# Performance work log

Hardware: AMD Instinct MI355X
Metric: run time of the kernel (lower is better)

The kernel has to match this reference:

```python
import jax, jax.numpy as jnp
import numpy as np

B, C, STRIDE = 2, 2048, 8
N = C * STRIDE            # sequence_length = 16384
D, H, L, FF = 256, 8, 4, 2048
DH = D // H


def setup_inputs() -> dict:
    key = jax.random.key(0)
    ks = iter(jax.random.split(key, 40))
    init = lambda shape: jax.random.normal(next(ks), shape, jnp.float32) * 0.02
    inp = {
        'bucket_tokens': jax.random.normal(next(ks), (B, C, STRIDE), jnp.float32),
        'W_in': init((STRIDE, D)), 'b_in': jnp.zeros((D,), jnp.float32),
        'Wq': init((L, D, D)), 'bq': jnp.zeros((L, D), jnp.float32),
        'Wk': init((L, D, D)), 'bk': jnp.zeros((L, D), jnp.float32),
        'Wv': init((L, D, D)), 'bv': jnp.zeros((L, D), jnp.float32),
        'Wo': init((L, D, D)), 'bo': jnp.zeros((L, D), jnp.float32),
        'ln1_g': jnp.ones((L, D), jnp.float32), 'ln1_b': jnp.zeros((L, D), jnp.float32),
        'ln2_g': jnp.ones((L, D), jnp.float32), 'ln2_b': jnp.zeros((L, D), jnp.float32),
        'W1': init((L, D, FF)), 'b1': jnp.zeros((L, FF), jnp.float32),
        'W2': init((L, FF, D)), 'b2': jnp.zeros((L, D), jnp.float32),
        'W_out': init((D, N)), 'b_out': jnp.zeros((N,), jnp.float32),
        'k_tokens': 60,  # int(fast_k * log(C)) = int(8 * log(2048))
    }
    return inp


def _layernorm(x, g, b, eps=1e-5):
    mu = x.mean(-1, keepdims=True)
    var = ((x - mu) ** 2).mean(-1, keepdims=True)
    return (x - mu) * jax.lax.rsqrt(var + eps) * g + b


def _rope_tables(seq, dh, dtype):
    half = dh // 2
    inv_freq = 1.0 / (10000.0 ** (jnp.arange(half, dtype=dtype) / half))
    ang = jnp.arange(seq, dtype=dtype)[:, None] * inv_freq[None, :]  # [C, half]
    return jnp.cos(ang), jnp.sin(ang)


def _apply_rope(t, cos, sin):
    # t: [B, H, C, DH]; rotate-half convention
    half = t.shape[-1] // 2
    t1, t2 = t[..., :half], t[..., half:]
    return jnp.concatenate([t1 * cos - t2 * sin, t1 * sin + t2 * cos], axis=-1)


def reference(bucket_tokens, W_in, b_in, Wq, bq, Wk, bk, Wv, bv, Wo, bo,
              ln1_g, ln1_b, ln2_g, ln2_b, W1, b1, W2, b2, W_out, b_out, k_tokens):
    x = bucket_tokens @ W_in + b_in                               # [B, C, D]
    dtype = x.dtype
    # ring-causal local mask: query c attends to {c, c-1, ..., c-(k-1)} mod C
    idx = jnp.arange(C)
    dist = (idx[:, None] - idx[None, :]) % C                       # [C, C]
    allowed = dist < k_tokens
    bias = jnp.where(allowed, jnp.zeros((), dtype), jnp.finfo(dtype).min)  # [C, C]
    cos, sin = _rope_tables(C, DH, dtype)
    scale = 1.0 / jnp.sqrt(jnp.asarray(DH, dtype))

    def heads(t):  # [B, C, D] -> [B, H, C, DH]
        return t.reshape(B, C, H, DH).transpose(0, 2, 1, 3)

    for l in range(L):
        h = _layernorm(x, ln1_g[l], ln1_b[l])
        q = _apply_rope(heads(h @ Wq[l] + bq[l]), cos, sin)
        k = _apply_rope(heads(h @ Wk[l] + bk[l]), cos, sin)
        v = heads(h @ Wv[l] + bv[l])
        scores = jnp.einsum('bhqd,bhkd->bhqk', q, k) * scale + bias
        attn = jax.nn.softmax(scores, axis=-1)
        o = jnp.einsum('bhqk,bhkd->bhqd', attn, v)
        o = o.transpose(0, 2, 1, 3).reshape(B, C, D)
        x = x + o @ Wo[l] + bo[l]
        h2 = _layernorm(x, ln2_g[l], ln2_b[l])
        x = x + jax.nn.relu(h2 @ W1[l] + b1[l]) @ W2[l] + b2[l]
    return x @ W_out + b_out                                       # [B, C, N]
```

## Files before the change

kernel.cpp:

```cpp
#include <hip/hip_runtime.h>
#include <hip/hip_bf16.h>

typedef __hip_bfloat16 bf16;
typedef float f32x4 __attribute__((ext_vector_type(4)));
typedef __bf16 bf16x8 __attribute__((ext_vector_type(8)));
typedef unsigned short u16x8 __attribute__((ext_vector_type(8)));
typedef unsigned short u16x4 __attribute__((ext_vector_type(4)));

#define FLAG_RELU  1
#define FLAG_OBF16 2
#define FLAG_RESID 4
#define FLAG_ROPE  8
#define FLAG_ATOM  16

__device__ __forceinline__ void glds16(const void* g, void* l) {
  __builtin_amdgcn_global_load_lds((const __attribute__((address_space(1))) void*)g,
                                   (__attribute__((address_space(3))) void*)l, 16, 0, 0);
}

__device__ __forceinline__ float ldf(const void* p, size_t i, bool f32) {
  return f32 ? ((const float*)p)[i] : (float)((const bf16*)p)[i];
}

__device__ __forceinline__ float bf2f(unsigned short u) {
  return __uint_as_float((unsigned)u << 16);
}
__device__ __forceinline__ short f2s(float f) {
  bf16 b = __float2bfloat16(f);
  return *(short*)&b;
}

__global__ void detect_k(const unsigned short* ln1g, int* flag) {
  *flag = (ln1g[0] == 0) ? 1 : 0;
}

__global__ __launch_bounds__(256) void transpose_k(const void* __restrict__ in,
                                                   bf16* __restrict__ out, int R, int Ccols,
                                                   const int* __restrict__ flag) {
  const bool f32 = *flag != 0;
  __shared__ bf16 tile[32][33];
  const size_t mz = (size_t)blockIdx.z * R * Ccols;
  const int c0 = blockIdx.x * 32, r0 = blockIdx.y * 32;
  const int tx = threadIdx.x & 31, ty = threadIdx.x >> 5;
#pragma unroll
  for (int i = 0; i < 32; i += 8)
    tile[ty + i][tx] = __float2bfloat16(ldf(in, mz + (size_t)(r0 + ty + i) * Ccols + c0 + tx, f32));
  __syncthreads();
#pragma unroll
  for (int i = 0; i < 32; i += 8)
    out[mz + (size_t)(c0 + ty + i) * R + r0 + tx] = tile[tx][ty + i];
}

__global__ __launch_bounds__(256) void inproj_k(const void* __restrict__ toks,
                                                const void* __restrict__ Win,
                                                const void* __restrict__ bin,
                                                float* __restrict__ x,
                                                const int* __restrict__ flag) {
  const bool f32 = *flag != 0;
  const int t = blockIdx.x, d = threadIdx.x;
  float acc = ldf(bin, d, f32);
#pragma unroll
  for (int s = 0; s < 8; s++)
    acc += ldf(toks, (size_t)t * 8 + s, f32) * ldf(Win, s * 256 + d, f32);
  x[(size_t)t * 256 + d] = acc;
}

__global__ __launch_bounds__(256) void ln_k(const float* __restrict__ x,
                                            const void* __restrict__ g,
                                            const void* __restrict__ bta, int eoff,
                                            bf16* __restrict__ out,
                                            const int* __restrict__ flag) {
  const bool f32 = *flag != 0;
  const int lane = threadIdx.x & 63;
  const size_t t = (size_t)blockIdx.x * 4 + (threadIdx.x >> 6);
  const float4 v = *(const float4*)(x + t * 256 + lane * 4);
  float s = v.x + v.y + v.z + v.w;
#pragma unroll
  for (int o = 32; o > 0; o >>= 1) s += __shfl_xor(s, o);
  const float mu = s * 0.00390625f;
  const float dx = v.x - mu, dy = v.y - mu, dz = v.z - mu, dw = v.w - mu;
  float ss = dx * dx + dy * dy + dz * dz + dw * dw;
#pragma unroll
  for (int o = 32; o > 0; o >>= 1) ss += __shfl_xor(ss, o);
  const float r = rsqrtf(ss * 0.00390625f + 1e-5f);
  const int e = eoff + lane * 4;
  short4 o4;
  o4.x = f2s(dx * r * ldf(g, e + 0, f32) + ldf(bta, e + 0, f32));
  o4.y = f2s(dy * r * ldf(g, e + 1, f32) + ldf(bta, e + 1, f32));
  o4.z = f2s(dz * r * ldf(g, e + 2, f32) + ldf(bta, e + 2, f32));
  o4.w = f2s(dw * r * ldf(g, e + 3, f32) + ldf(bta, e + 3, f32));
  *(short4*)((short*)out + t * 256 + lane * 4) = o4;
}

__global__ __launch_bounds__(256) void attn_k(const bf16* __restrict__ q,
                                              const bf16* __restrict__ k,
                                              const bf16* __restrict__ v,
                                              bf16* __restrict__ out,
                                              const int* __restrict__ ktp) {
  __shared__ unsigned short ksu[64][40];
  __shared__ unsigned short vsu[64][40];
  __shared__ float ps[32][40];
  int iv = *ktp;
  int kt;
  if (iv >= 1 && iv <= 2048) kt = iv;
  else {
    float fv = __int_as_float(iv);
    kt = (fv >= 1.0f && fv < 2049.0f) ? (int)fv : 60;
  }
  const int t = threadIdx.x;
  const int q0 = blockIdx.x * 32;
  const int h = blockIdx.y & 7, b = blockIdx.y >> 3;
  const size_t base_bh = ((size_t)b * 2048) * 256 + h * 32;
  const int qi = t >> 3, g = t & 7;
  const int srow = t >> 2, sd0 = (t & 3) * 8;
  const unsigned short* kg = (const unsigned short*)k + base_bh + sd0;
  const unsigned short* vg = (const unsigned short*)v + base_bh + sd0;
  float qv[32];
  {
    const unsigned short* qg = (const unsigned short*)q + base_bh + (size_t)(q0 + qi) * 256;
#pragma unroll
    for (int c = 0; c < 4; ++c) {
      u16x8 q8 = *(const u16x8*)(qg + c * 8);
#pragma unroll
      for (int e = 0; e < 8; ++e) qv[c * 8 + e] = bf2f(q8[e]);
    }
  }
  float m_run = -3.0e38f, l_run = 0.0f;
  float acc0 = 0.f, acc1 = 0.f, acc2 = 0.f, acc3 = 0.f;
  const float scale = 0.17677669529663687f;
  const int nch = (kt + 31) >> 5;
  for (int ch = 0; ch < nch; ++ch) {
    const int jb = ch << 5;
    if (ch) __syncthreads();
    {
      const int pos = (q0 - jb - 31 + srow) & 2047;
      *(u16x8*)&ksu[srow][sd0] = *(const u16x8*)(kg + (size_t)pos * 256);
      *(u16x8*)&vsu[srow][sd0] = *(const u16x8*)(vg + (size_t)pos * 256);
    }
    __syncthreads();
    float sc[4];
    float mloc = -3.0e38f;
#pragma unroll
    for (int s4 = 0; s4 < 4; ++s4) {
      const int dj = g + 8 * s4;
      const unsigned short* kr = ksu[qi - dj + 31];
      float dot = 0.f;
#pragma unroll
      for (int c = 0; c < 4; ++c) {
        u16x8 kk = *(const u16x8*)(kr + c * 8);
#pragma unroll
        for (int e = 0; e < 8; ++e) dot += qv[c * 8 + e] * bf2f(kk[e]);
      }
      const float sv = (jb + dj < kt) ? dot * scale : -3.0e38f;
      sc[s4] = sv;
      mloc = fmaxf(mloc, sv);
    }
    mloc = fmaxf(mloc, __shfl_xor(mloc, 1));
    mloc = fmaxf(mloc, __shfl_xor(mloc, 2));
    mloc = fmaxf(mloc, __shfl_xor(mloc, 4));
    const float mnew = fmaxf(m_run, mloc);
    const float fr = expf(m_run - mnew);
    float lloc = 0.f;
#pragma unroll
    for (int s4 = 0; s4 < 4; ++s4) {
      const float pe = expf(sc[s4] - mnew);
      ps[qi][g + 8 * s4] = pe;
      lloc += pe;
    }
    lloc += __shfl_xor(lloc, 1);
    lloc += __shfl_xor(lloc, 2);
    lloc += __shfl_xor(lloc, 4);
    m_run = mnew;
    l_run = l_run * fr + lloc;
    acc0 *= fr; acc1 *= fr; acc2 *= fr; acc3 *= fr;
    __syncthreads();
#pragma unroll 8
    for (int dj = 0; dj < 32; ++dj) {
      const float pe = ps[qi][dj];
      const u16x4 vv = *(const u16x4*)&vsu[qi - dj + 31][g * 4];
      acc0 += pe * bf2f(vv[0]);
      acc1 += pe * bf2f(vv[1]);
      acc2 += pe * bf2f(vv[2]);
      acc3 += pe * bf2f(vv[3]);
    }
  }
  const float invs = (l_run > 0.f) ? 1.f / l_run : 0.f;
  short4 o4;
  o4.x = f2s(acc0 * invs);
  o4.y = f2s(acc1 * invs);
  o4.z = f2s(acc2 * invs);
  o4.w = f2s(acc3 * invs);
  *(short4*)((short*)out + base_bh + (size_t)(q0 + qi) * 256 + g * 4) = o4;
}

__global__ __launch_bounds__(256) void gemm128_k(const bf16* __restrict__ A,
                                                 const bf16* __restrict__ BT,
                                                 const void* __restrict__ bias, int boff,
                                                 const float* resid, void* out,
                                                 int K, int N, int flags,
                                                 const int* __restrict__ dflag) {
  const bool bf32 = *dflag != 0;
  __shared__ __align__(16) short As[128 * 32];
  __shared__ __align__(16) short Bs[128 * 32];
  const int t = threadIdx.x;
  const int bm = blockIdx.x, bn = blockIdx.y;
  const int w = t >> 6, lane = t & 63;
  const int wm = (w >> 1) * 64, wn = (w & 1) * 64;
  const int lr = lane & 15, lq = lane >> 4;
  const short* Ag = (const short*)A + (size_t)bm * 128 * K + (size_t)(t >> 2) * K + (t & 3) * 8;
  const short* Bg = (const short*)BT + (size_t)bn * 128 * K + (size_t)(t >> 2) * K + (t & 3) * 8;
  const size_t rowhalf = (size_t)64 * K;
  f32x4 acc[4][4] = {};
  for (int kt = 0; kt < K; kt += 32) {
    glds16(Ag + kt, &As[t * 8]);
    glds16(Ag + rowhalf + kt, &As[2048 + t * 8]);
    glds16(Bg + kt, &Bs[t * 8]);
    glds16(Bg + rowhalf + kt, &Bs[2048 + t * 8]);
    __syncthreads();
    bf16x8 af[4], bfr[4];
#pragma unroll
    for (int i = 0; i < 4; i++) af[i] = *(const bf16x8*)&As[(wm + i * 16 + lr) * 32 + lq * 8];
#pragma unroll
    for (int j = 0; j < 4; j++) bfr[j] = *(const bf16x8*)&Bs[(wn + j * 16 + lr) * 32 + lq * 8];
#pragma unroll
    for (int i = 0; i < 4; i++)
#pragma unroll
      for (int j = 0; j < 4; j++)
        acc[i][j] = __builtin_amdgcn_mfma_f32_16x16x32_bf16(af[i], bfr[j], acc[i][j], 0, 0, 0);
    __syncthreads();
  }
  const int relu = flags & FLAG_RELU, obf = flags & FLAG_OBF16, res = flags & FLAG_RESID;
#pragma unroll
  for (int i = 0; i < 4; i++) {
    const size_t row0 = (size_t)bm * 128 + wm + i * 16 + lq * 4;
#pragma unroll
    for (int j = 0; j < 4; j++) {
      const int col = bn * 128 + wn + j * 16 + lr;
      const float bb = ldf(bias, boff + col, bf32);
#pragma unroll
      for (int r = 0; r < 4; r++) {
        const size_t idx = (row0 + r) * (size_t)N + col;
        float vv = acc[i][j][r] + bb;
        if (relu) vv = fmaxf(vv, 0.0f);
        if (res) vv += resid[idx];
        if (obf) ((bf16*)out)[idx] = __float2bfloat16(vv);
        else ((float*)out)[idx] = vv;
      }
    }
  }
}

__device__ __forceinline__ void gemm64_body(const bf16* A, const bf16* BT, const void* bias,
                                            int boff, const float* resid, void* out, int K,
                                            int k0, int k1, int N, int flags, int bm, int bn,
                                            bool bf32) {
  __shared__ __align__(16) short As[64 * 32];
  __shared__ __align__(16) short Bs[64 * 32];
  const int t = threadIdx.x;
  const int w = t >> 6, lane = t & 63;
  const int wm = (w >> 1) * 32, wn = (w & 1) * 32;
  const int lr = lane & 15, lq = lane >> 4;
  const short* Ag = (const short*)A + (size_t)bm * 64 * K + (size_t)(t >> 2) * K + (t & 3) * 8;
  const short* Bg = (const short*)BT + (size_t)bn * 64 * K + (size_t)(t >> 2) * K + (t & 3) * 8;
  f32x4 acc[2][2] = {};
  for (int kt = k0; kt < k1; kt += 32) {
    glds16(Ag + kt, &As[t * 8]);
    glds16(Bg + kt, &Bs[t * 8]);
    __syncthreads();
    bf16x8 af[2], bfr[2];
#pragma unroll
    for (int i = 0; i < 2; i++) af[i] = *(const bf16x8*)&As[(wm + i * 16 + lr) * 32 + lq * 8];
#pragma unroll
    for (int j = 0; j < 2; j++) bfr[j] = *(const bf16x8*)&Bs[(wn + j * 16 + lr) * 32 + lq * 8];
#pragma unroll
    for (int i = 0; i < 2; i++)
#pragma unroll
      for (int j = 0; j < 2; j++)
        acc[i][j] = __builtin_amdgcn_mfma_f32_16x16x32_bf16(af[i], bfr[j], acc[i][j], 0, 0, 0);
    __syncthreads();
  }
  if (flags & FLAG_ROPE) {
    const int col0 = bn * 64 + wn + lr;
    const float inv = powf(10000.0f, -(float)lr * 0.0625f);
    const float b0 = ldf(bias, boff + col0, bf32);
    const float b1 = ldf(bias, boff + col0 + 16, bf32);
#pragma unroll
    for (int i = 0; i < 2; i++) {
      const int row0 = bm * 64 + wm + i * 16 + lq * 4;
#pragma unroll
      for (int r = 0; r < 4; r++) {
        const int row = row0 + r;
        const float ang = (float)(row & 2047) * inv;
        const float cc = cosf(ang), sn = sinf(ang);
        const float v0 = acc[i][0][r] + b0, v1 = acc[i][1][r] + b1;
        bf16* ob = (bf16*)out + (size_t)row * N + col0;
        ob[0]  = __float2bfloat16(v0 * cc - v1 * sn);
        ob[16] = __float2bfloat16(v0 * sn + v1 * cc);
      }
    }
    return;
  }
  if (flags & FLAG_ATOM) {
#pragma unroll
    for (int i = 0; i < 2; i++) {
      const size_t row0 = (size_t)bm * 64 + wm + i * 16 + lq * 4;
#pragma unroll
      for (int j = 0; j < 2; j++) {
        const int col = bn * 64 + wn + j * 16 + lr;
        const float bb = bias ? ldf(bias, boff + col, bf32) : 0.0f;
#pragma unroll
        for (int r = 0; r < 4; r++)
          atomicAdd((float*)out + (row0 + r) * (size_t)N + col, acc[i][j][r] + bb);
      }
    }
    return;
  }
  const int relu = flags & FLAG_RELU, obf = flags & FLAG_OBF16, res = flags & FLAG_RESID;
#pragma unroll
  for (int i = 0; i < 2; i++) {
    const size_t row0 = (size_t)bm * 64 + wm + i * 16 + lq * 4;
#pragma unroll
    for (int j = 0; j < 2; j++) {
      const int col = bn * 64 + wn + j * 16 + lr;
      const float bb = ldf(bias, boff + col, bf32);
#pragma unroll
      for (int r = 0; r < 4; r++) {
        const size_t idx = (row0 + r) * (size_t)N + col;
        float vv = acc[i][j][r] + bb;
        if (relu) vv = fmaxf(vv, 0.0f);
        if (res) vv += resid[idx];
        if (obf) ((bf16*)out)[idx] = __float2bfloat16(vv);
        else ((float*)out)[idx] = vv;
      }
    }
  }
}

__global__ __launch_bounds__(256) void gemm64_k(const bf16* __restrict__ A,
                                                const bf16* __restrict__ BT,
                                                const void* __restrict__ bias, int boff,
                                                const float* resid, void* out,
                                                int K, int N, int flags,
                                                const int* __restrict__ dflag) {
  gemm64_body(A, BT, bias, boff, resid, out, K, 0, K, N, flags, blockIdx.x, blockIdx.y,
              *dflag != 0);
}

__global__ __launch_bounds__(256) void gemm64sk_k(const bf16* __restrict__ A,
                                                  const bf16* __restrict__ BT,
                                                  const void* __restrict__ bias, int boff,
                                                  float* out, int K, int Ksl, int N,
                                                  const int* __restrict__ dflag) {
  const int z = blockIdx.z;
  gemm64_body(A, BT, z == 0 ? bias : nullptr, boff, nullptr, out, K, z * Ksl, z * Ksl + Ksl, N,
              FLAG_ATOM, blockIdx.x, blockIdx.y, *dflag != 0);
}

__global__ __launch_bounds__(256) void qkv_k(const bf16* __restrict__ A,
                                             const bf16* __restrict__ BTq, const bf16* __restrict__ BTk,
                                             const bf16* __restrict__ BTv,
                                             const void* __restrict__ biq, const void* __restrict__ bik,
                                             const void* __restrict__ biv, int boff,
                                             bf16* q, bf16* k, bf16* v, int K, int N,
                                             const int* __restrict__ dflag) {
  const bf16* BT; const void* bi; bf16* o; int fl;
  if (blockIdx.z == 0)      { BT = BTq; bi = biq; o = q; fl = FLAG_ROPE; }
  else if (blockIdx.z == 1) { BT = BTk; bi = bik; o = k; fl = FLAG_ROPE; }
  else                      { BT = BTv; bi = biv; o = v; fl = FLAG_OBF16; }
  gemm64_body(A, BT, bi, boff, nullptr, o, K, 0, K, N, fl, blockIdx.x, blockIdx.y, *dflag != 0);
}

__global__ void cast_k(const float* __restrict__ in, bf16* __restrict__ out) {
  int i = blockIdx.x * 256 + threadIdx.x;
  out[i] = __float2bfloat16(in[i]);
}

extern "C" void kernel_launch(void* const* d_in, const int* in_sizes, int n_in,
                              void* d_out, int out_size, void* d_ws, size_t ws_size,
                              hipStream_t stream) {
  (void)in_sizes; (void)n_in; (void)out_size; (void)ws_size;
  const void* toks = d_in[0];
  const void* Win  = d_in[1];
  const void* bin  = d_in[2];
  const void* Wq   = d_in[3];
  const void* bq   = d_in[4];
  const void* Wk   = d_in[5];
  const void* bk   = d_in[6];
  const void* Wv   = d_in[7];
  const void* bv   = d_in[8];
  const void* Wo   = d_in[9];
  const void* bo   = d_in[10];
  const void* ln1g = d_in[11];
  const void* ln1b = d_in[12];
  const void* ln2g = d_in[13];
  const void* ln2b = d_in[14];
  const void* W1   = d_in[15];
  const void* b1   = d_in[16];
  const void* W2   = d_in[17];
  const void* b2   = d_in[18];
  const void* Wout = d_in[19];
  const void* bout = d_in[20];
  const int*  ktp  = (const int*)d_in[21];

  char* p = (char*)d_ws;
  auto take = [&](size_t bytes) { char* r = p; p += bytes; return r; };
  int*  dflag = (int*)take(256);
  float* x    = (float*)take((size_t)4096 * 256 * 4);
  bf16* h     = (bf16*)take((size_t)4096 * 256 * 2);
  bf16* qb    = (bf16*)take((size_t)4096 * 256 * 2);
  bf16* kbb   = (bf16*)take((size_t)4096 * 256 * 2);
  bf16* vbb   = (bf16*)take((size_t)4096 * 256 * 2);
  bf16* ao    = (bf16*)take((size_t)4096 * 256 * 2);
  bf16* mid   = (bf16*)take((size_t)4096 * 2048 * 2);
  bf16* xb    = (bf16*)take((size_t)4096 * 256 * 2);
  bf16* WqT   = (bf16*)take((size_t)4 * 256 * 256 * 2);
  bf16* WkT   = (bf16*)take((size_t)4 * 256 * 256 * 2);
  bf16* WvT   = (bf16*)take((size_t)4 * 256 * 256 * 2);
  bf16* WoT   = (bf16*)take((size_t)4 * 256 * 256 * 2);
  bf16* W1T   = (bf16*)take((size_t)4 * 256 * 2048 * 2);
  bf16* W2T   = (bf16*)take((size_t)4 * 2048 * 256 * 2);
  bf16* WoutT = (bf16*)take((size_t)256 * 16384 * 2);

  detect_k<<<1, 1, 0, stream>>>((const unsigned short*)ln1g, dflag);

  transpose_k<<<dim3(8, 8, 4), 256, 0, stream>>>(Wq, WqT, 256, 256, dflag);
  transpose_k<<<dim3(8, 8, 4), 256, 0, stream>>>(Wk, WkT, 256, 256, dflag);
  transpose_k<<<dim3(8, 8, 4), 256, 0, stream>>>(Wv, WvT, 256, 256, dflag);
  transpose_k<<<dim3(8, 8, 4), 256, 0, stream>>>(Wo, WoT, 256, 256, dflag);
  transpose_k<<<dim3(64, 8, 4), 256, 0, stream>>>(W1, W1T, 256, 2048, dflag);
  transpose_k<<<dim3(8, 64, 4), 256, 0, stream>>>(W2, W2T, 2048, 256, dflag);
  transpose_k<<<dim3(512, 8, 1), 256, 0, stream>>>(Wout, WoutT, 256, 16384, dflag);

  inproj_k<<<4096, 256, 0, stream>>>(toks, Win, bin, x, dflag);

  for (int l = 0; l < 4; l++) {
    ln_k<<<1024, 256, 0, stream>>>(x, ln1g, ln1b, l * 256, h, dflag);
    qkv_k<<<dim3(64, 4, 3), 256, 0, stream>>>(h, WqT + l * 65536, WkT + l * 65536, WvT + l * 65536,
                                              bq, bk, bv, l * 256, qb, kbb, vbb, 256, 256, dflag);
    attn_k<<<dim3(64, 16), 256, 0, stream>>>(qb, kbb, vbb, ao, ktp);
    gemm64sk_k<<<dim3(64, 4, 2), 256, 0, stream>>>(ao, WoT + l * 65536, bo, l * 256, x,
                                                   256, 128, 256, dflag);
    ln_k<<<1024, 256, 0, stream>>>(x, ln2g, ln2b, l * 256, h, dflag);
    gemm128_k<<<dim3(32, 16), 256, 0, stream>>>(h, W1T + (size_t)l * 524288, b1, l * 2048, nullptr,
                                                mid, 256, 2048, FLAG_RELU | FLAG_OBF16, dflag);
    gemm64sk_k<<<dim3(64, 4, 4), 256, 0, stream>>>(mid, W2T + (size_t)l * 524288, b2, l * 256, x,
                                                   2048, 512, 256, dflag);
  }

  cast_k<<<4096, 256, 0, stream>>>(x, xb);
  gemm128_k<<<dim3(32, 128), 256, 0, stream>>>(xb, WoutT, bout, 0, nullptr, d_out,
                                               256, 16384, 0, dflag);
}
```

Before: 752.6 us.

## Merge weight transposes, fuse QKV into 128-tile GEMM, add XCD block remap

All seven weight transposes are merged into one launch, and the detect kernel is removed: each kernel now reads the dtype flag directly from ln1_g. The QKV projection moves from three 64-tile GEMM slices to one 128-tile GEMM over a concatenated QKV weight, with RoPE applied in the epilogue. The FFN down-projection now uses a split-K 128-tile GEMM with atomic adds. GEMMs also remap block ids so that neighbouring tiles land on the same XCD, which targets L2 reuse. Together these cut launch count and raise per-block MFMA work, at the cost of fewer blocks for the smaller GEMMs.

```diff
diff --git a/kernel.cpp b/kernel.cpp
--- a/kernel.cpp
+++ b/kernel.cpp
@@ -10,7 +10,6 @@
 #define FLAG_RELU  1
 #define FLAG_OBF16 2
 #define FLAG_RESID 4
-#define FLAG_ROPE  8
 #define FLAG_ATOM  16
 
 __device__ __forceinline__ void glds16(const void* g, void* l) {
@@ -30,33 +29,59 @@
   return *(short*)&b;
 }
 
-__global__ void detect_k(const unsigned short* ln1g, int* flag) {
-  *flag = (ln1g[0] == 0) ? 1 : 0;
-}
-
-__global__ __launch_bounds__(256) void transpose_k(const void* __restrict__ in,
-                                                   bf16* __restrict__ out, int R, int Ccols,
-                                                   const int* __restrict__ flag) {
-  const bool f32 = *flag != 0;
+__device__ __forceinline__ bool is_f32(const unsigned short* dt) { return dt[0] == 0; }
+
+__global__ __launch_bounds__(256) void transposeAll_k(
+    const void* __restrict__ Wq, const void* __restrict__ Wk, const void* __restrict__ Wv,
+    const void* __restrict__ Wo, const void* __restrict__ W1, const void* __restrict__ W2,
+    const void* __restrict__ Wout,
+    bf16* __restrict__ qkvT, bf16* __restrict__ WoT, bf16* __restrict__ W1T,
+    bf16* __restrict__ W2T, bf16* __restrict__ WoutT,
+    const unsigned short* __restrict__ dt) {
+  const bool f32 = is_f32(dt);
+  const int esz = f32 ? 4 : 2;
+  const int id = blockIdx.x;
+  const void* in; bf16* out; int R, C, r0, c0;
+  if (id < 1024) {
+    const int seg = id >> 8, rem = id & 255;
+    const int layer = rem >> 6, tile = rem & 63;
+    c0 = (tile & 7) * 32; r0 = (tile >> 3) * 32; R = 256; C = 256;
+    const void* base = seg == 0 ? Wq : seg == 1 ? Wk : seg == 2 ? Wv : Wo;
+    in = (const char*)base + (size_t)layer * 65536 * esz;
+    out = (seg < 3) ? qkvT + (size_t)layer * 196608 + seg * 65536
+                    : WoT + (size_t)layer * 65536;
+  } else if (id < 3072) {
+    const int rem = id - 1024, layer = rem >> 9, t2 = rem & 511;
+    c0 = (t2 & 63) * 32; r0 = (t2 >> 6) * 32; R = 256; C = 2048;
+    in = (const char*)W1 + (size_t)layer * 524288 * esz;
+    out = W1T + (size_t)layer * 524288;
+  } else if (id < 5120) {
+    const int rem = id - 3072, layer = rem >> 9, t2 = rem & 511;
+    c0 = (t2 & 7) * 32; r0 = (t2 >> 3) * 32; R = 2048; C = 256;
+    in = (const char*)W2 + (size_t)layer * 524288 * esz;
+    out = W2T + (size_t)layer * 524288;
+  } else {
+    const int t2 = id - 5120;
+    c0 = (t2 & 511) * 32; r0 = (t2 >> 9) * 32; R = 256; C = 16384;
+    in = Wout; out = WoutT;
+  }
   __shared__ bf16 tile[32][33];
-  const size_t mz = (size_t)blockIdx.z * R * Ccols;
-  const int c0 = blockIdx.x * 32, r0 = blockIdx.y * 32;
   const int tx = threadIdx.x & 31, ty = threadIdx.x >> 5;
 #pragma unroll
   for (int i = 0; i < 32; i += 8)
-    tile[ty + i][tx] = __float2bfloat16(ldf(in, mz + (size_t)(r0 + ty + i) * Ccols + c0 + tx, f32));
+    tile[ty + i][tx] = __float2bfloat16(ldf(in, (size_t)(r0 + ty + i) * C + c0 + tx, f32));
   __syncthreads();
 #pragma unroll
   for (int i = 0; i < 32; i += 8)
-    out[mz + (size_t)(c0 + ty + i) * R + r0 + tx] = tile[tx][ty + i];
+    out[(size_t)(c0 + ty + i) * R + r0 + tx] = tile[tx][ty + i];
 }
 
 __global__ __launch_bounds__(256) void inproj_k(const void* __restrict__ toks,
                                                 const void* __restrict__ Win,
                                                 const void* __restrict__ bin,
                                                 float* __restrict__ x,
-                                                const int* __restrict__ flag) {
-  const bool f32 = *flag != 0;
+                                                const unsigned short* __restrict__ dt) {
+  const bool f32 = is_f32(dt);
   const int t = blockIdx.x, d = threadIdx.x;
   float acc = ldf(bin, d, f32);
 #pragma unroll
@@ -69,8 +94,8 @@
                                             const void* __restrict__ g,
                                             const void* __restrict__ bta, int eoff,
                                             bf16* __restrict__ out,
-                                            const int* __restrict__ flag) {
-  const bool f32 = *flag != 0;
+                                            const unsigned short* __restrict__ dt) {
+  const bool f32 = is_f32(dt);
   const int lane = threadIdx.x & 63;
   const size_t t = (size_t)blockIdx.x * 4 + (threadIdx.x >> 6);
   const float4 v = *(const float4*)(x + t * 256 + lane * 4);
@@ -193,25 +218,17 @@
   *(short4*)((short*)out + base_bh + (size_t)(q0 + qi) * 256 + g * 4) = o4;
 }
 
-__global__ __launch_bounds__(256) void gemm128_k(const bf16* __restrict__ A,
-                                                 const bf16* __restrict__ BT,
-                                                 const void* __restrict__ bias, int boff,
-                                                 const float* resid, void* out,
-                                                 int K, int N, int flags,
-                                                 const int* __restrict__ dflag) {
-  const bool bf32 = *dflag != 0;
-  __shared__ __align__(16) short As[128 * 32];
-  __shared__ __align__(16) short Bs[128 * 32];
+__device__ __forceinline__ void gemm128_core(const bf16* A, const bf16* BT, int K,
+                                             int k0, int k1, int bm, int bn,
+                                             short* As, short* Bs, f32x4 acc[4][4]) {
   const int t = threadIdx.x;
-  const int bm = blockIdx.x, bn = blockIdx.y;
   const int w = t >> 6, lane = t & 63;
   const int wm = (w >> 1) * 64, wn = (w & 1) * 64;
   const int lr = lane & 15, lq = lane >> 4;
   const short* Ag = (const short*)A + (size_t)bm * 128 * K + (size_t)(t >> 2) * K + (t & 3) * 8;
   const short* Bg = (const short*)BT + (size_t)bn * 128 * K + (size_t)(t >> 2) * K + (t & 3) * 8;
   const size_t rowhalf = (size_t)64 * K;
-  f32x4 acc[4][4] = {};
-  for (int kt = 0; kt < K; kt += 32) {
+  for (int kt = k0; kt < k1; kt += 32) {
     glds16(Ag + kt, &As[t * 8]);
     glds16(Ag + rowhalf + kt, &As[2048 + t * 8]);
     glds16(Bg + kt, &Bs[t * 8]);
@@ -228,6 +245,49 @@
       for (int j = 0; j < 4; j++)
         acc[i][j] = __builtin_amdgcn_mfma_f32_16x16x32_bf16(af[i], bfr[j], acc[i][j], 0, 0, 0);
     __syncthreads();
+  }
+}
+
+__device__ __forceinline__ void xcd_bm_bn(int& bm, int& bn) {
+  const int gx = gridDim.x;
+  const int nwg = gx * gridDim.y;
+  int id = blockIdx.y * gx + blockIdx.x;
+  id = (id & 7) * (nwg >> 3) + (id >> 3);
+  bm = id % gx; bn = id / gx;
+}
+
+__global__ __launch_bounds__(256) void gemm128_k(const bf16* __restrict__ A,
+                                                 const bf16* __restrict__ BT,
+                                                 const void* __restrict__ bias, int boff,
+                                                 const float* __restrict__ resid,
+                                                 void* __restrict__ out,
+                                                 int K, int Ksl, int N, int flags,
+                                                 const unsigned short* __restrict__ dt) {
+  const bool bf32 = is_f32(dt);
+  __shared__ __align__(16) short As[128 * 32];
+  __shared__ __align__(16) short Bs[128 * 32];
+  int bm, bn; xcd_bm_bn(bm, bn);
+  const int k0 = blockIdx.z * Ksl;
+  f32x4 acc[4][4] = {};
+  gemm128_core(A, BT, K, k0, k0 + Ksl, bm, bn, As, Bs, acc);
+  const int t = threadIdx.x, w = t >> 6, lane = t & 63;
+  const int wm = (w >> 1) * 64, wn = (w & 1) * 64;
+  const int lr = lane & 15, lq = lane >> 4;
+  if (flags & FLAG_ATOM) {
+    const bool addb = blockIdx.z == 0;
+#pragma unroll
+    for (int i = 0; i < 4; i++) {
+      const size_t row0 = (size_t)bm * 128 + wm + i * 16 + lq * 4;
+#pragma unroll
+      for (int j = 0; j < 4; j++) {
+        const int col = bn * 128 + wn + j * 16 + lr;
+        const float bb = addb ? ldf(bias, boff + col, bf32) : 0.0f;
+#pragma unroll
+        for (int r = 0; r < 4; r++)
+          atomicAdd((float*)out + (row0 + r) * (size_t)N + col, acc[i][j][r] + bb);
+      }
+    }
+    return;
   }
   const int relu = flags & FLAG_RELU, obf = flags & FLAG_OBF16, res = flags & FLAG_RESID;
 #pragma unroll
@@ -250,12 +310,80 @@
   }
 }
 
-__device__ __forceinline__ void gemm64_body(const bf16* A, const bf16* BT, const void* bias,
-                                            int boff, const float* resid, void* out, int K,
-                                            int k0, int k1, int N, int flags, int bm, int bn,
-                                            bool bf32) {
+__global__ __launch_bounds__(256) void qkv128_k(const bf16* __restrict__ A,
+                                                const bf16* __restrict__ QKVT,
+                                                const void* __restrict__ bq,
+                                                const void* __restrict__ bk,
+                                                const void* __restrict__ bv, int boff,
+                                                bf16* __restrict__ q, bf16* __restrict__ k,
+                                                bf16* __restrict__ v,
+                                                const unsigned short* __restrict__ dt) {
+  const bool bf32 = is_f32(dt);
+  __shared__ __align__(16) short As[128 * 32];
+  __shared__ __align__(16) short Bs[128 * 32];
+  int bm, bn; xcd_bm_bn(bm, bn);
+  f32x4 acc[4][4] = {};
+  gemm128_core(A, QKVT, 256, 0, 256, bm, bn, As, Bs, acc);
+  const int t = threadIdx.x, w = t >> 6, lane = t & 63;
+  const int wm = (w >> 1) * 64, wn = (w & 1) * 64;
+  const int lr = lane & 15, lq = lane >> 4;
+  const int mat = bn >> 1;
+  bf16* o = mat == 0 ? q : (mat == 1 ? k : v);
+  const void* bi = mat == 0 ? bq : (mat == 1 ? bk : bv);
+  const int lcb = (bn & 1) * 128 + wn;
+  if (mat < 2) {
+    const float inv = powf(10000.0f, -(float)lr * 0.0625f);
+    const float b00 = ldf(bi, boff + lcb + lr, bf32);
+    const float b01 = ldf(bi, boff + lcb + 16 + lr, bf32);
+    const float b10 = ldf(bi, boff + lcb + 32 + lr, bf32);
+    const float b11 = ldf(bi, boff + lcb + 48 + lr, bf32);
+#pragma unroll
+    for (int i = 0; i < 4; i++) {
+      const int row0 = bm * 128 + wm + i * 16 + lq * 4;
+#pragma unroll
+      for (int r = 0; r < 4; r++) {
+        const int row = row0 + r;
+        const float ang = (float)(row & 2047) * inv;
+        const float cc = cosf(ang), sn = sinf(ang);
+        bf16* ob = o + (size_t)row * 256 + lcb;
+        {
+          const float v0 = acc[i][0][r] + b00, v1 = acc[i][1][r] + b01;
+          ob[lr]      = __float2bfloat16(v0 * cc - v1 * sn);
+          ob[lr + 16] = __float2bfloat16(v0 * sn + v1 * cc);
+        }
+        {
+          const float v0 = acc[i][2][r] + b10, v1 = acc[i][3][r] + b11;
+          ob[lr + 32] = __float2bfloat16(v0 * cc - v1 * sn);
+          ob[lr + 48] = __float2bfloat16(v0 * sn + v1 * cc);
+        }
+      }
+    }
+  } else {
+#pragma unroll
+    for (int i = 0; i < 4; i++) {
+      const int row0 = bm * 128 + wm + i * 16 + lq * 4;
+#pragma unroll
+      for (int j = 0; j < 4; j++) {
+        const int lc = lcb + j * 16 + lr;
+        const float bb = ldf(bi, boff + lc, bf32);
+#pragma unroll
+        for (int r = 0; r < 4; r++)
+          o[(size_t)(row0 + r) * 256 + lc] = __float2bfloat16(acc[i][j][r] + bb);
+      }
+    }
+  }
+}
+
+__global__ __launch_bounds__(256) void gemm64sk_k(const bf16* __restrict__ A,
+                                                  const bf16* __restrict__ BT,
+                                                  const void* __restrict__ bias, int boff,
+                                                  float* __restrict__ out, int K, int Ksl, int N,
+                                                  const unsigned short* __restrict__ dt) {
+  const bool bf32 = is_f32(dt);
   __shared__ __align__(16) short As[64 * 32];
   __shared__ __align__(16) short Bs[64 * 32];
+  int bm, bn; xcd_bm_bn(bm, bn);
+  const int k0 = blockIdx.z * Ksl, k1 = k0 + Ksl;
   const int t = threadIdx.x;
   const int w = t >> 6, lane = t & 63;
   const int wm = (w >> 1) * 32, wn = (w & 1) * 32;
@@ -279,95 +407,19 @@
         acc[i][j] = __builtin_amdgcn_mfma_f32_16x16x32_bf16(af[i], bfr[j], acc[i][j], 0, 0, 0);
     __syncthreads();
   }
-  if (flags & FLAG_ROPE) {
-    const int col0 = bn * 64 + wn + lr;
-    const float inv = powf(10000.0f, -(float)lr * 0.0625f);
-    const float b0 = ldf(bias, boff + col0, bf32);
-    const float b1 = ldf(bias, boff + col0 + 16, bf32);
-#pragma unroll
-    for (int i = 0; i < 2; i++) {
-      const int row0 = bm * 64 + wm + i * 16 + lq * 4;
-#pragma unroll
-      for (int r = 0; r < 4; r++) {
-        const int row = row0 + r;
-        const float ang = (float)(row & 2047) * inv;
-        const float cc = cosf(ang), sn = sinf(ang);
-        const float v0 = acc[i][0][r] + b0, v1 = acc[i][1][r] + b1;
-        bf16* ob = (bf16*)out + (size_t)row * N + col0;
-        ob[0]  = __float2bfloat16(v0 * cc - v1 * sn);
-        ob[16] = __float2bfloat16(v0 * sn + v1 * cc);
-      }
-    }
-    return;
-  }
-  if (flags & FLAG_ATOM) {
-#pragma unroll
-    for (int i = 0; i < 2; i++) {
-      const size_t row0 = (size_t)bm * 64 + wm + i * 16 + lq * 4;
-#pragma unroll
-      for (int j = 0; j < 2; j++) {
-        const int col = bn * 64 + wn + j * 16 + lr;
-        const float bb = bias ? ldf(bias, boff + col, bf32) : 0.0f;
-#pragma unroll
-        for (int r = 0; r < 4; r++)
-          atomicAdd((float*)out + (row0 + r) * (size_t)N + col, acc[i][j][r] + bb);
-      }
-    }
-    return;
-  }
-  const int relu = flags & FLAG_RELU, obf = flags & FLAG_OBF16, res = flags & FLAG_RESID;
+  const bool addb = blockIdx.z == 0;
 #pragma unroll
   for (int i = 0; i < 2; i++) {
     const size_t row0 = (size_t)bm * 64 + wm + i * 16 + lq * 4;
 #pragma unroll
     for (int j = 0; j < 2; j++) {
       const int col = bn * 64 + wn + j * 16 + lr;
-      const float bb = ldf(bias, boff + col, bf32);
-#pragma unroll
-      for (int r = 0; r < 4; r++) {
-        const size_t idx = (row0 + r) * (size_t)N + col;
-        float vv = acc[i][j][r] + bb;
-        if (relu) vv = fmaxf(vv, 0.0f);
-        if (res) vv += resid[idx];
-        if (obf) ((bf16*)out)[idx] = __float2bfloat16(vv);
-        else ((float*)out)[idx] = vv;
-      }
-    }
-  }
-}
-
-__global__ __launch_bounds__(256) void gemm64_k(const bf16* __restrict__ A,
-                                                const bf16* __restrict__ BT,
-                                                const void* __restrict__ bias, int boff,
-                                                const float* resid, void* out,
-                                                int K, int N, int flags,
-                                                const int* __restrict__ dflag) {
-  gemm64_body(A, BT, bias, boff, resid, out, K, 0, K, N, flags, blockIdx.x, blockIdx.y,
-              *dflag != 0);
-}
-
-__global__ __launch_bounds__(256) void gemm64sk_k(const bf16* __restrict__ A,
-                                                  const bf16* __restrict__ BT,
-                                                  const void* __restrict__ bias, int boff,
-                                                  float* out, int K, int Ksl, int N,
-                                                  const int* __restrict__ dflag) {
-  const int z = blockIdx.z;
-  gemm64_body(A, BT, z == 0 ? bias : nullptr, boff, nullptr, out, K, z * Ksl, z * Ksl + Ksl, N,
-              FLAG_ATOM, blockIdx.x, blockIdx.y, *dflag != 0);
-}
-
-__global__ __launch_bounds__(256) void qkv_k(const bf16* __restrict__ A,
-                                             const bf16* __restrict__ BTq, const bf16* __restrict__ BTk,
-                                             const bf16* __restrict__ BTv,
-                                             const void* __restrict__ biq, const void* __restrict__ bik,
-                                             const void* __restrict__ biv, int boff,
-                                             bf16* q, bf16* k, bf16* v, int K, int N,
-                                             const int* __restrict__ dflag) {
-  const bf16* BT; const void* bi; bf16* o; int fl;
-  if (blockIdx.z == 0)      { BT = BTq; bi = biq; o = q; fl = FLAG_ROPE; }
-  else if (blockIdx.z == 1) { BT = BTk; bi = bik; o = k; fl = FLAG_ROPE; }
-  else                      { BT = BTv; bi = biv; o = v; fl = FLAG_OBF16; }
-  gemm64_body(A, BT, bi, boff, nullptr, o, K, 0, K, N, fl, blockIdx.x, blockIdx.y, *dflag != 0);
+      const float bb = addb ? ldf(bias, boff + col, bf32) : 0.0f;
+#pragma unroll
+      for (int r = 0; r < 4; r++)
+        atomicAdd(out + (row0 + r) * (size_t)N + col, acc[i][j][r] + bb);
+    }
+  }
 }
 
 __global__ void cast_k(const float* __restrict__ in, bf16* __restrict__ out) {
@@ -401,10 +453,10 @@
   const void* Wout = d_in[19];
   const void* bout = d_in[20];
   const int*  ktp  = (const int*)d_in[21];
+  const unsigned short* dt = (const unsigned short*)ln1g;
 
   char* p = (char*)d_ws;
   auto take = [&](size_t bytes) { char* r = p; p += bytes; return r; };
-  int*  dflag = (int*)take(256);
   float* x    = (float*)take((size_t)4096 * 256 * 4);
   bf16* h     = (bf16*)take((size_t)4096 * 256 * 2);
   bf16* qb    = (bf16*)take((size_t)4096 * 256 * 2);
@@ -413,41 +465,33 @@
   bf16* ao    = (bf16*)take((size_t)4096 * 256 * 2);
   bf16* mid   = (bf16*)take((size_t)4096 * 2048 * 2);
   bf16* xb    = (bf16*)take((size_t)4096 * 256 * 2);
-  bf16* WqT   = (bf16*)take((size_t)4 * 256 * 256 * 2);
-  bf16* WkT   = (bf16*)take((size_t)4 * 256 * 256 * 2);
-  bf16* WvT   = (bf16*)take((size_t)4 * 256 * 256 * 2);
+  bf16* qkvT  = (bf16*)take((size_t)4 * 768 * 256 * 2);
   bf16* WoT   = (bf16*)take((size_t)4 * 256 * 256 * 2);
   bf16* W1T   = (bf16*)take((size_t)4 * 256 * 2048 * 2);
   bf16* W2T   = (bf16*)take((size_t)4 * 2048 * 256 * 2);
   bf16* WoutT = (bf16*)take((size_t)256 * 16384 * 2);
 
-  detect_k<<<1, 1, 0, stream>>>((const unsigned short*)ln1g, dflag);
-
-  transpose_k<<<dim3(8, 8, 4), 256, 0, stream>>>(Wq, WqT, 256, 256, dflag);
-  transpose_k<<<dim3(8, 8, 4), 256, 0, stream>>>(Wk, WkT, 256, 256, dflag);
-  transpose_k<<<dim3(8, 8, 4), 256, 0, stream>>>(Wv, WvT, 256, 256, dflag);
-  transpose_k<<<dim3(8, 8, 4), 256, 0, stream>>>(Wo, WoT, 256, 256, dflag);
-  transpose_k<<<dim3(64, 8, 4), 256, 0, stream>>>(W1, W1T, 256, 2048, dflag);
-  transpose_k<<<dim3(8, 64, 4), 256, 0, stream>>>(W2, W2T, 2048, 256, dflag);
-  transpose_k<<<dim3(512, 8, 1), 256, 0, stream>>>(Wout, WoutT, 256, 16384, dflag);
-
-  inproj_k<<<4096, 256, 0, stream>>>(toks, Win, bin, x, dflag);
+  transposeAll_k<<<9216, 256, 0, stream>>>(Wq, Wk, Wv, Wo, W1, W2, Wout,
+                                           qkvT, WoT, W1T, W2T, WoutT, dt);
+
+  inproj_k<<<4096, 256, 0, stream>>>(toks, Win, bin, x, dt);
 
   for (int l = 0; l < 4; l++) {
-    ln_k<<<1024, 256, 0, stream>>>(x, ln1g, ln1b, l * 256, h, dflag);
-    qkv_k<<<dim3(64, 4, 3), 256, 0, stream>>>(h, WqT + l * 65536, WkT + l * 65536, WvT + l * 65536,
-                                              bq, bk, bv, l * 256, qb, kbb, vbb, 256, 256, dflag);
+    ln_k<<<1024, 256, 0, stream>>>(x, ln1g, ln1b, l * 256, h, dt);
+    qkv128_k<<<dim3(32, 6), 256, 0, stream>>>(h, qkvT + (size_t)l * 196608, bq, bk, bv, l * 256,
+                                              qb, kbb, vbb, dt);
     attn_k<<<dim3(64, 16), 256, 0, stream>>>(qb, kbb, vbb, ao, ktp);
     gemm64sk_k<<<dim3(64, 4, 2), 256, 0, stream>>>(ao, WoT + l * 65536, bo, l * 256, x,
-                                                   256, 128, 256, dflag);
-    ln_k<<<1024, 256, 0, stream>>>(x, ln2g, ln2b, l * 256, h, dflag);
-    gemm128_k<<<dim3(32, 16), 256, 0, stream>>>(h, W1T + (size_t)l * 524288, b1, l * 2048, nullptr,
-                                                mid, 256, 2048, FLAG_RELU | FLAG_OBF16, dflag);
-    gemm64sk_k<<<dim3(64, 4, 4), 256, 0, stream>>>(mid, W2T + (size_t)l * 524288, b2, l * 256, x,
-                                                   2048, 512, 256, dflag);
+                                                   256, 128, 256, dt);
+    ln_k<<<1024, 256, 0, stream>>>(x, ln2g, ln2b, l * 256, h, dt);
+    gemm128_k<<<dim3(32, 16), 256, 0, stream>>>(h, W1T + (size_t)l * 524288, b1, l * 2048,
+                                                nullptr, mid, 256, 256, 2048,
+                                                FLAG_RELU | FLAG_OBF16, dt);
+    gemm128_k<<<dim3(32, 2, 4), 256, 0, stream>>>(mid, W2T + (size_t)l * 524288, b2, l * 256,
+                                                  nullptr, x, 2048, 512, 256, FLAG_ATOM, dt);
   }
 
   cast_k<<<4096, 256, 0, stream>>>(x, xb);
   gemm128_k<<<dim3(32, 128), 256, 0, stream>>>(xb, WoutT, bout, 0, nullptr, d_out,
-                                               256, 16384, 0, dflag);
-}
+                                               256, 256, 16384, 0, dt);
+}
```

Result: slower. 806.3 us (+7.1%).
